# Optimization experiments

Hardware: AMD Instinct MI355X
Metric: run time of the kernel (lower is better)

The kernel has to match this reference:

```python
import jax, jax.numpy as jnp
import numpy as np

N_NODES = 100000
N_EDGES = 625000
D_IN = 128
D_OUT = 128
N_ETYPES = 64


def setup_inputs() -> dict:
    key = jax.random.key(0)
    k1, k2, k3, k4, k5, k6 = jax.random.split(key, 6)
    node_features = jax.random.normal(k1, (N_NODES, D_IN), dtype=jnp.float32)
    edge_index = jax.random.randint(k2, (2, N_EDGES), 0, N_NODES, dtype=jnp.int64)
    edge_type = jax.random.randint(k3, (N_EDGES,), 0, N_ETYPES, dtype=jnp.int64)
    edge_emb = jax.random.normal(k4, (N_ETYPES, D_OUT), dtype=jnp.float32)
    W = jax.random.normal(k5, (D_IN, D_OUT), dtype=jnp.float32) / np.sqrt(D_IN)
    b = jax.random.normal(k6, (D_OUT,), dtype=jnp.float32) * 0.01
    return {"node_features": node_features, "edge_index": edge_index,
            "edge_type": edge_type, "edge_emb": edge_emb, "W": W, "b": b}


def reference(node_features, edge_index, edge_type, edge_emb, W, b):
    # Linear transform of node features: (N, D_out)
    h = node_features @ W + b
    src, tgt = edge_index[0], edge_index[1]
    # Per-edge message: gather src feature + edge-type embedding  (E, D_out)
    messages = h[src] + edge_emb[edge_type]
    # Scatter-add into target nodes
    aggregated = jax.ops.segment_sum(messages, tgt, num_segments=N_NODES)
    # Self contribution + ReLU
    return jax.nn.relu(aggregated + h)
```

## Files before the change

kernel.cpp:

```cpp
#include <hip/hip_runtime.h>
#include <hip/hip_bf16.h>

#define D 128

typedef __attribute__((ext_vector_type(8))) short short8v;
typedef __attribute__((ext_vector_type(4))) float float4v;

__device__ __forceinline__ unsigned short f2bf(float f) {
  union { float f; unsigned int u; } v; v.f = f;
  unsigned int r = v.u + 0x7fffu + ((v.u >> 16) & 1u);
  return (unsigned short)(r >> 16);
}
__device__ __forceinline__ float bf2f(unsigned int bits16) {
  union { unsigned int u; float f; } v; v.u = bits16 << 16;
  return v.f;
}

__global__ __launch_bounds__(256) void wt_prep_kernel(
    const float* __restrict__ W, unsigned short* __restrict__ Wt) {
  int i = blockIdx.x * 256 + threadIdx.x;
  if (i < D * D) Wt[i] = f2bf(W[(i & 127) * D + (i >> 7)]);
}

#define XS_STRIDE 136
__global__ __launch_bounds__(256) void gemm_h_kernel(
    const float* __restrict__ nf, const unsigned short* __restrict__ Wt,
    const float* __restrict__ b, unsigned short* __restrict__ h_bf,
    int n_nodes) {
  __shared__ unsigned short Xs[32 * XS_STRIDE];
  const int tid = threadIdx.x;
  const int nodeBase = blockIdx.x * 32;

  #pragma unroll
  for (int s = 0; s < 2; ++s) {
    const int row = (tid >> 4) + s * 16;
    const int col = (tid & 15) * 8;
    const float4* p =
        (const float4*)&nf[(size_t)(nodeBase + row) * D + col];
    float4 a = p[0], c = p[1];
    short8v sv;
    sv[0] = (short)f2bf(a.x); sv[1] = (short)f2bf(a.y);
    sv[2] = (short)f2bf(a.z); sv[3] = (short)f2bf(a.w);
    sv[4] = (short)f2bf(c.x); sv[5] = (short)f2bf(c.y);
    sv[6] = (short)f2bf(c.z); sv[7] = (short)f2bf(c.w);
    *(short8v*)&Xs[row * XS_STRIDE + col] = sv;
  }

  const int w = tid >> 6;
  const int l = tid & 63;
  const int m = l & 15;
  const int q = l >> 4;
  const int r0 = (w & 1) * 16;
  const int c0 = (w >> 1) * 64;

  short8v bfrag[4][4];
  float bias[4];
  #pragma unroll
  for (int ct = 0; ct < 4; ++ct) {
    const int n = c0 + ct * 16 + m;
    bias[ct] = b[n];
    #pragma unroll
    for (int kc = 0; kc < 4; ++kc)
      bfrag[ct][kc] = *(const short8v*)&Wt[n * D + kc * 32 + q * 8];
  }

  float4v acc[4] = {{0,0,0,0},{0,0,0,0},{0,0,0,0},{0,0,0,0}};
  __syncthreads();

  #pragma unroll
  for (int kc = 0; kc < 4; ++kc) {
    const short8v av =
        *(const short8v*)&Xs[(r0 + m) * XS_STRIDE + kc * 32 + q * 8];
    #pragma unroll
    for (int ct = 0; ct < 4; ++ct)
      acc[ct] = __builtin_amdgcn_mfma_f32_16x16x32_bf16(av, bfrag[ct][kc],
                                                        acc[ct], 0, 0, 0);
  }

  #pragma unroll
  for (int ct = 0; ct < 4; ++ct) {
    const int col = c0 + ct * 16 + m;
    #pragma unroll
    for (int r = 0; r < 4; ++r) {
      const int node = nodeBase + r0 + q * 4 + r;
      h_bf[(size_t)node * D + col] = f2bf(acc[ct][r] + bias[ct]);
    }
  }
}

__global__ __launch_bounds__(256) void hist_kernel(
    const int* __restrict__ eidx, int* __restrict__ counts, int n_edges) {
  int e = blockIdx.x * 256 + threadIdx.x;
  if (e < n_edges) atomicAdd(&counts[eidx[n_edges + e]], 1);
}

__global__ __launch_bounds__(256) void scan1_kernel(
    const int* __restrict__ counts, int* __restrict__ offsets,
    int* __restrict__ blockSums, int n) {
  __shared__ int lds[256];
  const int tid = threadIdx.x;
  const int base = blockIdx.x * 1024 + tid * 4;
  int v[4];
  #pragma unroll
  for (int k = 0; k < 4; ++k) v[k] = (base + k < n) ? counts[base + k] : 0;
  int s = v[0] + v[1] + v[2] + v[3];
  lds[tid] = s;
  for (int off = 1; off < 256; off <<= 1) {
    __syncthreads();
    int t = (tid >= off) ? lds[tid - off] : 0;
    __syncthreads();
    lds[tid] += t;
  }
  __syncthreads();
  int run = lds[tid] - s;
  #pragma unroll
  for (int k = 0; k < 4; ++k) {
    if (base + k < n) offsets[base + k] = run;
    run += v[k];
  }
  if (tid == 255) blockSums[blockIdx.x] = lds[255];
}

__global__ __launch_bounds__(1024) void scan2_kernel(int* __restrict__ blockSums,
                                                     int* __restrict__ blockOffs,
                                                     int nb) {
  __shared__ int lds[1024];
  const int tid = threadIdx.x;
  int v = (tid < nb) ? blockSums[tid] : 0;
  lds[tid] = v;
  for (int off = 1; off < 1024; off <<= 1) {
    __syncthreads();
    int t = (tid >= off) ? lds[tid - off] : 0;
    __syncthreads();
    lds[tid] += t;
  }
  __syncthreads();
  if (tid < nb) blockOffs[tid] = lds[tid] - v;
}

__global__ __launch_bounds__(256) void scan3_kernel(
    int* __restrict__ offsets, int* __restrict__ cursor,
    const int* __restrict__ blockOffs, int n, int n_edges) {
  const int tid = threadIdx.x;
  const int add = blockOffs[blockIdx.x];
  const int base = blockIdx.x * 1024 + tid * 4;
  #pragma unroll
  for (int k = 0; k < 4; ++k) {
    int i = base + k;
    if (i < n) {
      int o = offsets[i] + add;
      offsets[i] = o;
      cursor[i] = o;
    }
  }
  if (blockIdx.x == 0 && tid == 0) offsets[n] = n_edges;
}

__global__ __launch_bounds__(256) void scatter_kernel(
    const int* __restrict__ eidx, const int* __restrict__ etype,
    int* __restrict__ cursor, unsigned int* __restrict__ packed, int n_edges) {
  int e = blockIdx.x * 256 + threadIdx.x;
  if (e >= n_edges) return;
  const int src = eidx[e];
  const int tgt = eidx[n_edges + e];
  const int et = etype[e];
  const int pos = atomicAdd(&cursor[tgt], 1);
  packed[pos] = (unsigned int)src | ((unsigned int)et << 17);
}

__global__ __launch_bounds__(256) void aggregate_kernel(
    const int* __restrict__ offsets, const unsigned int* __restrict__ packed,
    const float* __restrict__ eemb, const unsigned int* __restrict__ h2,
    float* __restrict__ out, int n_nodes) {
  const int gid = blockIdx.x * 256 + threadIdx.x;
  const int n = gid >> 6;
  const int lane = gid & 63;
  if (n >= n_nodes) return;

  const float2* e2 = (const float2*)eemb;

  const unsigned int sb = h2[n * 64 + lane];
  float ax = bf2f(sb & 0xffffu), ay = bf2f(sb >> 16);

  int j = offsets[n];
  const int end = offsets[n + 1];
  for (; j + 1 < end; j += 2) {
    const unsigned int p0 = packed[j];
    const unsigned int p1 = packed[j + 1];
    const unsigned int g0 = h2[(p0 & 0x1FFFFu) * 64 + lane];
    const unsigned int g1 = h2[(p1 & 0x1FFFFu) * 64 + lane];
    const float2 e0 = e2[(p0 >> 17) * 64 + lane];
    const float2 e1 = e2[(p1 >> 17) * 64 + lane];
    ax += bf2f(g0 & 0xffffu) + e0.x + bf2f(g1 & 0xffffu) + e1.x;
    ay += bf2f(g0 >> 16) + e0.y + bf2f(g1 >> 16) + e1.y;
  }
  if (j < end) {
    const unsigned int p0 = packed[j];
    const unsigned int g0 = h2[(p0 & 0x1FFFFu) * 64 + lane];
    const float2 e0 = e2[(p0 >> 17) * 64 + lane];
    ax += bf2f(g0 & 0xffffu) + e0.x;
    ay += bf2f(g0 >> 16) + e0.y;
  }
  float2 r;
  r.x = fmaxf(ax, 0.f);
  r.y = fmaxf(ay, 0.f);
  ((float2*)out)[(size_t)n * 64 + lane] = r;
}

extern "C" void kernel_launch(void* const* d_in, const int* in_sizes, int n_in,
                              void* d_out, int out_size, void* d_ws,
                              size_t ws_size, hipStream_t stream) {
  const float* nf   = (const float*)d_in[0];
  const int*   eidx = (const int*)d_in[1];
  const int*   etyp = (const int*)d_in[2];
  const float* eemb = (const float*)d_in[3];
  const float* W    = (const float*)d_in[4];
  const float* b    = (const float*)d_in[5];

  const int n_nodes = in_sizes[0] / D;
  const int n_edges = in_sizes[2];

  float* out = (float*)d_out;

  char* base = (char*)d_ws;
  unsigned short* Wt = (unsigned short*)base;
  unsigned short* h_bf = (unsigned short*)(base + 32768);
  int* counts = (int*)(base + 32768 + (size_t)n_nodes * D * 2);
  int* offsets = counts + n_nodes;
  int* cursor = offsets + (n_nodes + 1);
  int* blockSums = cursor + n_nodes;
  int* blockOffs = blockSums + 1024;
  unsigned int* packed = (unsigned int*)(blockOffs + 1024);

  const int nb = (n_nodes + 1023) / 1024;

  wt_prep_kernel<<<64, 256, 0, stream>>>(W, Wt);

  gemm_h_kernel<<<(n_nodes + 31) / 32, 256, 0, stream>>>(nf, Wt, b, h_bf,
                                                         n_nodes);

  hipMemsetAsync(counts, 0, (size_t)n_nodes * 4, stream);
  hist_kernel<<<(n_edges + 255) / 256, 256, 0, stream>>>(eidx, counts, n_edges);
  scan1_kernel<<<nb, 256, 0, stream>>>(counts, offsets, blockSums, n_nodes);
  scan2_kernel<<<1, 1024, 0, stream>>>(blockSums, blockOffs, nb);
  scan3_kernel<<<nb, 256, 0, stream>>>(offsets, cursor, blockOffs, n_nodes,
                                       n_edges);
  scatter_kernel<<<(n_edges + 255) / 256, 256, 0, stream>>>(eidx, etyp, cursor,
                                                            packed, n_edges);

  const long long aggThreads = (long long)n_nodes * 64;
  aggregate_kernel<<<(int)((aggThreads + 255) / 256), 256, 0, stream>>>(
      offsets, packed, eemb, (const unsigned int*)h_bf, out, n_nodes);
}
```

Before: 161.1 us.

## Store edge embeddings as bf16, unroll aggregation by four, retile GEMM to 64 nodes

Edge-type embeddings are converted to bf16 in the prep kernel, which halves the per-edge embedding gather traffic in the aggregation kernel. The aggregation loop is unrolled by four with two independent accumulators to keep more loads in flight. The GEMM now processes 64 nodes per block with swapped operands, so each thread writes packed 8-byte h stores instead of scattered 2-byte stores, and tail rows are bounds-checked. Rounding the embeddings to bf16 adds a small numeric error to every message.

```diff
diff --git a/kernel.cpp b/kernel.cpp
--- a/kernel.cpp
+++ b/kernel.cpp
@@ -16,33 +16,38 @@
   return v.f;
 }
 
-__global__ __launch_bounds__(256) void wt_prep_kernel(
-    const float* __restrict__ W, unsigned short* __restrict__ Wt) {
+__global__ __launch_bounds__(256) void prep_kernel(
+    const float* __restrict__ W, const float* __restrict__ eemb,
+    unsigned short* __restrict__ Wt, unsigned short* __restrict__ em_bf) {
   int i = blockIdx.x * 256 + threadIdx.x;
   if (i < D * D) Wt[i] = f2bf(W[(i & 127) * D + (i >> 7)]);
-}
-
-#define XS_STRIDE 136
+  if (i < 64 * D) em_bf[i] = f2bf(eemb[i]);
+}
+
+#define XS_STRIDE 138
 __global__ __launch_bounds__(256) void gemm_h_kernel(
     const float* __restrict__ nf, const unsigned short* __restrict__ Wt,
     const float* __restrict__ b, unsigned short* __restrict__ h_bf,
     int n_nodes) {
-  __shared__ unsigned short Xs[32 * XS_STRIDE];
-  const int tid = threadIdx.x;
-  const int nodeBase = blockIdx.x * 32;
-
-  #pragma unroll
-  for (int s = 0; s < 2; ++s) {
+  __shared__ unsigned short Xs[64 * XS_STRIDE];
+  const int tid = threadIdx.x;
+  const int nodeBase = blockIdx.x * 64;
+
+  #pragma unroll
+  for (int s = 0; s < 4; ++s) {
     const int row = (tid >> 4) + s * 16;
     const int col = (tid & 15) * 8;
-    const float4* p =
-        (const float4*)&nf[(size_t)(nodeBase + row) * D + col];
-    float4 a = p[0], c = p[1];
     short8v sv;
-    sv[0] = (short)f2bf(a.x); sv[1] = (short)f2bf(a.y);
-    sv[2] = (short)f2bf(a.z); sv[3] = (short)f2bf(a.w);
-    sv[4] = (short)f2bf(c.x); sv[5] = (short)f2bf(c.y);
-    sv[6] = (short)f2bf(c.z); sv[7] = (short)f2bf(c.w);
+    if (nodeBase + row < n_nodes) {
+      const float4* p = (const float4*)&nf[(size_t)(nodeBase + row) * D + col];
+      float4 a = p[0], c = p[1];
+      sv[0] = (short)f2bf(a.x); sv[1] = (short)f2bf(a.y);
+      sv[2] = (short)f2bf(a.z); sv[3] = (short)f2bf(a.w);
+      sv[4] = (short)f2bf(c.x); sv[5] = (short)f2bf(c.y);
+      sv[6] = (short)f2bf(c.z); sv[7] = (short)f2bf(c.w);
+    } else {
+      sv = short8v{0, 0, 0, 0, 0, 0, 0, 0};
+    }
     *(short8v*)&Xs[row * XS_STRIDE + col] = sv;
   }
 
@@ -50,40 +55,50 @@
   const int l = tid & 63;
   const int m = l & 15;
   const int q = l >> 4;
-  const int r0 = (w & 1) * 16;
-  const int c0 = (w >> 1) * 64;
-
-  short8v bfrag[4][4];
-  float bias[4];
-  #pragma unroll
-  for (int ct = 0; ct < 4; ++ct) {
-    const int n = c0 + ct * 16 + m;
-    bias[ct] = b[n];
+  const int n0 = (w & 1) * 64;
+  const int nodeHalf = (w >> 1) * 32;
+
+  short8v afrag[4][4];
+  #pragma unroll
+  for (int nt = 0; nt < 4; ++nt) {
+    const int n = n0 + nt * 16 + m;
     #pragma unroll
     for (int kc = 0; kc < 4; ++kc)
-      bfrag[ct][kc] = *(const short8v*)&Wt[n * D + kc * 32 + q * 8];
-  }
-
-  float4v acc[4] = {{0,0,0,0},{0,0,0,0},{0,0,0,0},{0,0,0,0}};
+      afrag[nt][kc] = *(const short8v*)&Wt[n * D + kc * 32 + q * 8];
+  }
+
+  float4v acc[4][2] = {};
   __syncthreads();
 
   #pragma unroll
   for (int kc = 0; kc < 4; ++kc) {
-    const short8v av =
-        *(const short8v*)&Xs[(r0 + m) * XS_STRIDE + kc * 32 + q * 8];
     #pragma unroll
-    for (int ct = 0; ct < 4; ++ct)
-      acc[ct] = __builtin_amdgcn_mfma_f32_16x16x32_bf16(av, bfrag[ct][kc],
-                                                        acc[ct], 0, 0, 0);
-  }
-
-  #pragma unroll
-  for (int ct = 0; ct < 4; ++ct) {
-    const int col = c0 + ct * 16 + m;
+    for (int t = 0; t < 2; ++t) {
+      const int node = nodeHalf + t * 16 + m;
+      const short8v bv =
+          *(const short8v*)&Xs[node * XS_STRIDE + kc * 32 + q * 8];
+      #pragma unroll
+      for (int nt = 0; nt < 4; ++nt)
+        acc[nt][t] = __builtin_amdgcn_mfma_f32_16x16x32_bf16(
+            afrag[nt][kc], bv, acc[nt][t], 0, 0, 0);
+    }
+  }
+
+  #pragma unroll
+  for (int nt = 0; nt < 4; ++nt) {
+    const int colBase = n0 + nt * 16 + q * 4;
+    const float4 bv = *(const float4*)&b[colBase];
     #pragma unroll
-    for (int r = 0; r < 4; ++r) {
-      const int node = nodeBase + r0 + q * 4 + r;
-      h_bf[(size_t)node * D + col] = f2bf(acc[ct][r] + bias[ct]);
+    for (int t = 0; t < 2; ++t) {
+      const int node = nodeBase + nodeHalf + t * 16 + m;
+      if (node < n_nodes) {
+        const unsigned int lo = (unsigned int)f2bf(acc[nt][t][0] + bv.x) |
+                                ((unsigned int)f2bf(acc[nt][t][1] + bv.y) << 16);
+        const unsigned int hi = (unsigned int)f2bf(acc[nt][t][2] + bv.z) |
+                                ((unsigned int)f2bf(acc[nt][t][3] + bv.w) << 16);
+        uint2 val; val.x = lo; val.y = hi;
+        *(uint2*)&h_bf[(size_t)node * D + colBase] = val;
+      }
     }
   }
 }
@@ -170,40 +185,51 @@
 
 __global__ __launch_bounds__(256) void aggregate_kernel(
     const int* __restrict__ offsets, const unsigned int* __restrict__ packed,
-    const float* __restrict__ eemb, const unsigned int* __restrict__ h2,
+    const unsigned int* __restrict__ em, const unsigned int* __restrict__ h2,
     float* __restrict__ out, int n_nodes) {
   const int gid = blockIdx.x * 256 + threadIdx.x;
   const int n = gid >> 6;
   const int lane = gid & 63;
   if (n >= n_nodes) return;
 
-  const float2* e2 = (const float2*)eemb;
-
   const unsigned int sb = h2[n * 64 + lane];
-  float ax = bf2f(sb & 0xffffu), ay = bf2f(sb >> 16);
+  float ax0 = bf2f(sb & 0xffffu), ay0 = bf2f(sb >> 16);
+  float ax1 = 0.f, ay1 = 0.f;
 
   int j = offsets[n];
   const int end = offsets[n + 1];
-  for (; j + 1 < end; j += 2) {
+  for (; j + 3 < end; j += 4) {
     const unsigned int p0 = packed[j];
     const unsigned int p1 = packed[j + 1];
+    const unsigned int p2 = packed[j + 2];
+    const unsigned int p3 = packed[j + 3];
     const unsigned int g0 = h2[(p0 & 0x1FFFFu) * 64 + lane];
     const unsigned int g1 = h2[(p1 & 0x1FFFFu) * 64 + lane];
-    const float2 e0 = e2[(p0 >> 17) * 64 + lane];
-    const float2 e1 = e2[(p1 >> 17) * 64 + lane];
-    ax += bf2f(g0 & 0xffffu) + e0.x + bf2f(g1 & 0xffffu) + e1.x;
-    ay += bf2f(g0 >> 16) + e0.y + bf2f(g1 >> 16) + e1.y;
-  }
-  if (j < end) {
+    const unsigned int g2 = h2[(p2 & 0x1FFFFu) * 64 + lane];
+    const unsigned int g3 = h2[(p3 & 0x1FFFFu) * 64 + lane];
+    const unsigned int e0 = em[(p0 >> 17) * 64 + lane];
+    const unsigned int e1 = em[(p1 >> 17) * 64 + lane];
+    const unsigned int e2 = em[(p2 >> 17) * 64 + lane];
+    const unsigned int e3 = em[(p3 >> 17) * 64 + lane];
+    ax0 += bf2f(g0 & 0xffffu) + bf2f(e0 & 0xffffu);
+    ay0 += bf2f(g0 >> 16) + bf2f(e0 >> 16);
+    ax1 += bf2f(g1 & 0xffffu) + bf2f(e1 & 0xffffu);
+    ay1 += bf2f(g1 >> 16) + bf2f(e1 >> 16);
+    ax0 += bf2f(g2 & 0xffffu) + bf2f(e2 & 0xffffu);
+    ay0 += bf2f(g2 >> 16) + bf2f(e2 >> 16);
+    ax1 += bf2f(g3 & 0xffffu) + bf2f(e3 & 0xffffu);
+    ay1 += bf2f(g3 >> 16) + bf2f(e3 >> 16);
+  }
+  for (; j < end; ++j) {
     const unsigned int p0 = packed[j];
     const unsigned int g0 = h2[(p0 & 0x1FFFFu) * 64 + lane];
-    const float2 e0 = e2[(p0 >> 17) * 64 + lane];
-    ax += bf2f(g0 & 0xffffu) + e0.x;
-    ay += bf2f(g0 >> 16) + e0.y;
+    const unsigned int e0 = em[(p0 >> 17) * 64 + lane];
+    ax0 += bf2f(g0 & 0xffffu) + bf2f(e0 & 0xffffu);
+    ay0 += bf2f(g0 >> 16) + bf2f(e0 >> 16);
   }
   float2 r;
-  r.x = fmaxf(ax, 0.f);
-  r.y = fmaxf(ay, 0.f);
+  r.x = fmaxf(ax0 + ax1, 0.f);
+  r.y = fmaxf(ay0 + ay1, 0.f);
   ((float2*)out)[(size_t)n * 64 + lane] = r;
 }
 
@@ -224,8 +250,9 @@
 
   char* base = (char*)d_ws;
   unsigned short* Wt = (unsigned short*)base;
-  unsigned short* h_bf = (unsigned short*)(base + 32768);
-  int* counts = (int*)(base + 32768 + (size_t)n_nodes * D * 2);
+  unsigned short* em_bf = (unsigned short*)(base + 32768);
+  unsigned short* h_bf = (unsigned short*)(base + 49152);
+  int* counts = (int*)(base + 49152 + (size_t)n_nodes * D * 2);
   int* offsets = counts + n_nodes;
   int* cursor = offsets + (n_nodes + 1);
   int* blockSums = cursor + n_nodes;
@@ -234,12 +261,12 @@
 
   const int nb = (n_nodes + 1023) / 1024;
 
-  wt_prep_kernel<<<64, 256, 0, stream>>>(W, Wt);
-
-  gemm_h_kernel<<<(n_nodes + 31) / 32, 256, 0, stream>>>(nf, Wt, b, h_bf,
+  prep_kernel<<<64, 256, 0, stream>>>(W, eemb, Wt, em_bf);
+
+  gemm_h_kernel<<<(n_nodes + 63) / 64, 256, 0, stream>>>(nf, Wt, b, h_bf,
                                                          n_nodes);
 
-  hipMemsetAsync(counts, 0, (size_t)n_nodes * 4, stream);
+  (void)hipMemsetAsync(counts, 0, (size_t)n_nodes * 4, stream);
   hist_kernel<<<(n_edges + 255) / 256, 256, 0, stream>>>(eidx, counts, n_edges);
   scan1_kernel<<<nb, 256, 0, stream>>>(counts, offsets, blockSums, n_nodes);
   scan2_kernel<<<1, 1024, 0, stream>>>(blockSums, blockOffs, nb);
@@ -250,5 +277,6 @@
 
   const long long aggThreads = (long long)n_nodes * 64;
   aggregate_kernel<<<(int)((aggThreads + 255) / 256), 256, 0, stream>>>(
-      offsets, packed, eemb, (const unsigned int*)h_bf, out, n_nodes);
-}
+      offsets, packed, (const unsigned int*)em_bf, (const unsigned int*)h_bf,
+      out, n_nodes);
+}
```

Result: faster. 154.2 us (-4.3%).
